# Kernel optimization log

Hardware: AMD Instinct MI355X
Metric: run time of the kernel (lower is better)

Reference implementation:

```python
import jax, jax.numpy as jnp
import numpy as np

B, T, C, I, E, K, V, H = 4, 512, 512, 2048, 32, 2, 32000, 8
D = C // H
EPS = 1e-5


def setup_inputs() -> dict:
    key = jax.random.key(0)
    ks = jax.random.split(key, 16)
    s = 0.02
    inp = {
        "input_ids": jax.random.randint(ks[0], (B, T), 0, V),
        "emb": jax.random.normal(ks[1], (V, C), jnp.float32) * s,
        "wq": jax.random.normal(ks[2], (C, C), jnp.float32) * s,
        "wk": jax.random.normal(ks[3], (C, C), jnp.float32) * s,
        "wv": jax.random.normal(ks[4], (C, C), jnp.float32) * s,
        "wo": jax.random.normal(ks[5], (C, C), jnp.float32) * s,
        "gate": jax.random.normal(ks[6], (C, E), jnp.float32) * s,
        "w1": jax.random.normal(ks[7], (E, C, I), jnp.float32) * s,
        "w2": jax.random.normal(ks[8], (E, I, C), jnp.float32) * s,
        "g1": jnp.ones((C,), jnp.float32) + jax.random.normal(ks[9], (C,), jnp.float32) * 0.01,
        "b1": jax.random.normal(ks[10], (C,), jnp.float32) * 0.01,
        "g2": jnp.ones((C,), jnp.float32) + jax.random.normal(ks[11], (C,), jnp.float32) * 0.01,
        "b2": jax.random.normal(ks[12], (C,), jnp.float32) * 0.01,
        "lm_head": jax.random.normal(ks[13], (C, V), jnp.float32) * s,
    }
    return inp


def _ln(x, g, b):
    mu = jnp.mean(x, axis=-1, keepdims=True)
    var = jnp.mean(jnp.square(x - mu), axis=-1, keepdims=True)
    return (x - mu) * jax.lax.rsqrt(var + EPS) * g + b


def reference(input_ids, emb, wq, wk, wv, wo, gate, w1, w2, g1, b1, g2, b2, lm_head):
    h = emb[input_ids]  # [B,T,C]
    # --- attention block ---
    x = _ln(h, g1, b1)
    q = (x @ wq).reshape(B, T, H, D).transpose(0, 2, 1, 3)  # [B,H,T,D]
    k = (x @ wk).reshape(B, T, H, D).transpose(0, 2, 1, 3)
    v = (x @ wv).reshape(B, T, H, D).transpose(0, 2, 1, 3)
    scores = jnp.einsum('bhqd,bhkd->bhqk', q, k) / jnp.sqrt(jnp.float32(D))
    causal = jnp.tril(jnp.ones((T, T), bool))
    scores = jnp.where(causal, scores, jnp.finfo(scores.dtype).min)
    attn = jax.nn.softmax(scores, axis=-1)
    ao = jnp.einsum('bhqk,bhkd->bhqd', attn, v)
    ao = ao.transpose(0, 2, 1, 3).reshape(B, T, C) @ wo
    h = h + ao
    # --- MoE block ---
    x2 = _ln(h, g2, b2)          # hidden_states_for_moe [B,T,C]
    flat = x2.reshape(-1, C)     # [N,C], N = B*T tokens
    router_logits = flat @ gate  # [N,E]
    rw, sel = jax.lax.top_k(router_logits, K)   # [N,K]
    rw = jax.nn.softmax(rw.astype(jnp.float32), axis=-1)
    # dense per-expert FFN, then mask to selected experts (same math as
    # torch's loop: unselected (token,expert) slots stay zero)
    hidden = jax.nn.gelu(jnp.einsum('tc,eci->tei', flat, w1), approximate=False)
    all_out = jnp.einsum('tei,eic->tec', hidden, w2)  # [N,E,C]
    sel_mask = jnp.sum(jax.nn.one_hot(sel, E, dtype=all_out.dtype), axis=1)  # [N,E]
    full_expert_outputs = all_out * sel_mask[:, :, None]
    gathered = jnp.take_along_axis(full_expert_outputs, sel[:, :, None], axis=1)  # [N,K,C]
    moe_out = jnp.einsum('tk,tkc->tc', rw, gathered).reshape(B, T, C)
    h = h + moe_out
    logits = h @ lm_head
    return logits, full_expert_outputs, router_logits, x2
```

## Files before the change

kernel.cpp:

```cpp
#include <hip/hip_runtime.h>
#include <hip/hip_bf16.h>

#define BATCH 4
#define SEQ   512
#define CH    512
#define NTOK  2048
#define FF    2048
#define NEXP  32
#define TOPK  2
#define VOCAB 32000
#define NHEAD 8
#define HDIM  64
#define EPSF  1e-5f

typedef __attribute__((ext_vector_type(8))) short short8v;
typedef __attribute__((ext_vector_type(4))) float f32x4;

#define GLD16(g, lds) __builtin_amdgcn_global_load_lds(                      \
    (const __attribute__((address_space(1))) void*)(g),                      \
    (__attribute__((address_space(3))) void*)(lds), 16, 0, 0)

__device__ __forceinline__ unsigned short bf16r(float f) {
  unsigned int u = __float_as_uint(f);
  u = (u + 0x7FFFu + ((u >> 16) & 1u)) >> 16;
  return (unsigned short)u;
}

__device__ __forceinline__ float block_reduce_sum(float v, float* sbuf) {
  #pragma unroll
  for (int off = 32; off > 0; off >>= 1) v += __shfl_down(v, off, 64);
  const int lane = threadIdx.x & 63, wid = threadIdx.x >> 6;
  __syncthreads();
  if (lane == 0) sbuf[wid] = v;
  __syncthreads();
  return sbuf[0] + sbuf[1] + sbuf[2] + sbuf[3];
}

__device__ __forceinline__ float gelu_exact(float v) {
  return 0.5f * v * (1.f + erff(v * 0.70710678118654752f));
}

__global__ __launch_bounds__(256) void transpose_cvt_kernel(
    const float* __restrict__ in, unsigned short* __restrict__ out, int R, int C) {
  __shared__ float T[64][65];
  const size_t zoff = (size_t)blockIdx.z * R * C;
  in += zoff; out += zoff;
  const int r0 = blockIdx.y << 6;
  const int c0 = blockIdx.x << 6;
  const int t = threadIdx.x;
  const int lr = t >> 4;
  const int lc = (t & 15) << 2;
  #pragma unroll
  for (int rr = 0; rr < 64; rr += 16) {
    const float4 v = *(const float4*)(in + (size_t)(r0 + lr + rr) * C + c0 + lc);
    T[lr + rr][lc + 0] = v.x; T[lr + rr][lc + 1] = v.y;
    T[lr + rr][lc + 2] = v.z; T[lr + rr][lc + 3] = v.w;
  }
  __syncthreads();
  const int oc = t >> 2;
  const int rs = (t & 3) << 4;
  unsigned int pk[8];
  #pragma unroll
  for (int j = 0; j < 8; ++j) {
    const float a = T[rs + 2 * j][oc];
    const float b = T[rs + 2 * j + 1][oc];
    pk[j] = (unsigned int)bf16r(a) | ((unsigned int)bf16r(b) << 16);
  }
  unsigned short* op = out + (size_t)(c0 + oc) * R + r0 + rs;
  *(uint4*)(op)     = make_uint4(pk[0], pk[1], pk[2], pk[3]);
  *(uint4*)(op + 8) = make_uint4(pk[4], pk[5], pk[6], pk[7]);
}

__global__ __launch_bounds__(256) void embed_ln_kernel(
    const int* __restrict__ ids, const float* __restrict__ emb,
    const float* __restrict__ g, const float* __restrict__ b,
    float* __restrict__ h, float* __restrict__ x) {
  __shared__ float sbuf[4];
  const int n = blockIdx.x, t = threadIdx.x;
  const float2 v = *(const float2*)(emb + (size_t)ids[n] * CH + 2 * t);
  *(float2*)(h + (size_t)n * CH + 2 * t) = v;
  const float mu = block_reduce_sum(v.x + v.y, sbuf) * (1.f / CH);
  const float d0 = v.x - mu, d1 = v.y - mu;
  const float var = block_reduce_sum(d0 * d0 + d1 * d1, sbuf) * (1.f / CH);
  const float rstd = rsqrtf(var + EPSF);
  const float2 gg = *(const float2*)(g + 2 * t);
  const float2 bb = *(const float2*)(b + 2 * t);
  *(float2*)(x + (size_t)n * CH + 2 * t) =
      make_float2(d0 * rstd * gg.x + bb.x, d1 * rstd * gg.y + bb.y);
}

__global__ __launch_bounds__(256) void ln2_router_kernel(
    const float* __restrict__ in, const float* __restrict__ g,
    const float* __restrict__ b, const float* __restrict__ gate,
    float* __restrict__ outf, unsigned short* __restrict__ outbf,
    float* __restrict__ rl, float* __restrict__ rw, int* __restrict__ sel,
    int* __restrict__ counts, int* __restrict__ lists) {
  __shared__ float sbuf[4];
  __shared__ float xrow[CH];
  __shared__ float lg[NEXP];
  const int n = blockIdx.x, t = threadIdx.x;
  const float2 v = *(const float2*)(in + (size_t)n * CH + 2 * t);
  const float mu = block_reduce_sum(v.x + v.y, sbuf) * (1.f / CH);
  const float d0 = v.x - mu, d1 = v.y - mu;
  const float var = block_reduce_sum(d0 * d0 + d1 * d1, sbuf) * (1.f / CH);
  const float rstd = rsqrtf(var + EPSF);
  const float2 gg = *(const float2*)(g + 2 * t);
  const float2 bb = *(const float2*)(b + 2 * t);
  const float o0 = d0 * rstd * gg.x + bb.x;
  const float o1 = d1 * rstd * gg.y + bb.y;
  *(float2*)(outf + (size_t)n * CH + 2 * t) = make_float2(o0, o1);
  ((unsigned int*)outbf)[(size_t)n * (CH / 2) + t] =
      (unsigned int)bf16r(o0) | ((unsigned int)bf16r(o1) << 16);
  xrow[2 * t] = o0; xrow[2 * t + 1] = o1;
  __syncthreads();
  const int e = t >> 3, i = t & 7;
  float p = 0.f;
  const float* gp = gate + e;
  for (int c = i * 64; c < i * 64 + 64; ++c) p = fmaf(xrow[c], gp[(size_t)c * NEXP], p);
  p += __shfl_xor(p, 1, 64);
  p += __shfl_xor(p, 2, 64);
  p += __shfl_xor(p, 4, 64);
  if (i == 0) { lg[e] = p; rl[(size_t)n * NEXP + e] = p; }
  __syncthreads();
  if (t == 0) {
    int i0 = 0; float v0 = lg[0];
    for (int j = 1; j < NEXP; ++j) if (lg[j] > v0) { v0 = lg[j]; i0 = j; }
    int i1 = (i0 == 0) ? 1 : 0; float v1 = lg[i1];
    for (int j = 0; j < NEXP; ++j) {
      if (j == i0 || j == i1) continue;
      if (lg[j] > v1) { v1 = lg[j]; i1 = j; }
    }
    const float ex = expf(v1 - v0);
    const float den = 1.f + ex;
    rw[n * 2]     = 1.f / den;
    rw[n * 2 + 1] = ex / den;
    sel[n * 2]     = i0;
    sel[n * 2 + 1] = i1;
    const int s0 = atomicAdd(&counts[i0], 1);
    lists[i0 * NTOK + s0] = n * 2;
    const int s1 = atomicAdd(&counts[i1], 1);
    lists[i1 * NTOK + s1] = n * 2 + 1;
  }
}

__global__ __launch_bounds__(256) void gemm_f32_qkv_kernel(
    const float* __restrict__ A,
    const float* __restrict__ Wq, const float* __restrict__ Wk,
    const float* __restrict__ Wv,
    float* __restrict__ Oq, float* __restrict__ Ok, float* __restrict__ Ov,
    int M, int N, int K) {
  const float* B = (blockIdx.z == 0) ? Wq : (blockIdx.z == 1) ? Wk : Wv;
  float*       C = (blockIdx.z == 0) ? Oq : (blockIdx.z == 1) ? Ok : Ov;
  __shared__ float As[32][68];
  __shared__ float Bs[32][132];
  const int m0 = blockIdx.y << 6;
  const int n0 = blockIdx.x << 7;
  const int t  = threadIdx.x;
  const int tm = t >> 4;
  const int tn = t & 15;
  float acc[4][8];
  #pragma unroll
  for (int i = 0; i < 4; ++i)
    #pragma unroll
    for (int j = 0; j < 8; ++j) acc[i][j] = 0.f;

  const int ar = t >> 3;
  const int ac = (t & 7) << 2;
  const int bk = t >> 3;
  const int bn = (t & 7) << 4;

  for (int kt = 0; kt < K; kt += 32) {
    #pragma unroll
    for (int rr = 0; rr < 64; rr += 32) {
      float4 a = *(const float4*)(A + (size_t)(m0 + ar + rr) * K + kt + ac);
      As[ac + 0][ar + rr] = a.x; As[ac + 1][ar + rr] = a.y;
      As[ac + 2][ar + rr] = a.z; As[ac + 3][ar + rr] = a.w;
    }
    const float* bp = B + (size_t)(kt + bk) * N + n0 + bn;
    #pragma unroll
    for (int j = 0; j < 16; j += 4)
      *(float4*)&Bs[bk][bn + j] = *(const float4*)(bp + j);
    __syncthreads();
    #pragma unroll
    for (int k = 0; k < 32; ++k) {
      const float4 av = *(const float4*)&As[k][tm << 2];
      const float4 bl = *(const float4*)&Bs[k][tn << 2];
      const float4 bh = *(const float4*)&Bs[k][64 + (tn << 2)];
      const float a_[4] = {av.x, av.y, av.z, av.w};
      const float b_[8] = {bl.x, bl.y, bl.z, bl.w, bh.x, bh.y, bh.z, bh.w};
      #pragma unroll
      for (int i = 0; i < 4; ++i)
        #pragma unroll
        for (int j = 0; j < 8; ++j)
          acc[i][j] = fmaf(a_[i], b_[j], acc[i][j]);
    }
    __syncthreads();
  }
  #pragma unroll
  for (int i = 0; i < 4; ++i) {
    const int row = m0 + (tm << 2) + i;
    float* cp = C + (size_t)row * N + n0 + (tn << 2);
    *(float4*)cp        = make_float4(acc[i][0], acc[i][1], acc[i][2], acc[i][3]);
    *(float4*)(cp + 64) = make_float4(acc[i][4], acc[i][5], acc[i][6], acc[i][7]);
  }
}

__global__ __launch_bounds__(256) void gemm_f32_kernel(
    const float* __restrict__ A, const float* __restrict__ B,
    const float* __restrict__ Res, float* __restrict__ C,
    int M, int N, int K) {
  __shared__ float As[32][68];
  __shared__ float Bs[32][132];
  const int m0 = blockIdx.y << 6;
  const int n0 = blockIdx.x << 7;
  const int t  = threadIdx.x;
  const int tm = t >> 4;
  const int tn = t & 15;
  float acc[4][8];
  #pragma unroll
  for (int i = 0; i < 4; ++i)
    #pragma unroll
    for (int j = 0; j < 8; ++j) acc[i][j] = 0.f;

  const int ar = t >> 3;
  const int ac = (t & 7) << 2;
  const int bk = t >> 3;
  const int bn = (t & 7) << 4;

  for (int kt = 0; kt < K; kt += 32) {
    #pragma unroll
    for (int rr = 0; rr < 64; rr += 32) {
      float4 a = *(const float4*)(A + (size_t)(m0 + ar + rr) * K + kt + ac);
      As[ac + 0][ar + rr] = a.x; As[ac + 1][ar + rr] = a.y;
      As[ac + 2][ar + rr] = a.z; As[ac + 3][ar + rr] = a.w;
    }
    const float* bp = B + (size_t)(kt + bk) * N + n0 + bn;
    #pragma unroll
    for (int j = 0; j < 16; j += 4)
      *(float4*)&Bs[bk][bn + j] = *(const float4*)(bp + j);
    __syncthreads();
    #pragma unroll
    for (int k = 0; k < 32; ++k) {
      const float4 av = *(const float4*)&As[k][tm << 2];
      const float4 bl = *(const float4*)&Bs[k][tn << 2];
      const float4 bh = *(const float4*)&Bs[k][64 + (tn << 2)];
      const float a_[4] = {av.x, av.y, av.z, av.w};
      const float b_[8] = {bl.x, bl.y, bl.z, bl.w, bh.x, bh.y, bh.z, bh.w};
      #pragma unroll
      for (int i = 0; i < 4; ++i)
        #pragma unroll
        for (int j = 0; j < 8; ++j)
          acc[i][j] = fmaf(a_[i], b_[j], acc[i][j]);
    }
    __syncthreads();
  }
  #pragma unroll
  for (int i = 0; i < 4; ++i) {
    const int row = m0 + (tm << 2) + i;
    float* cp = C + (size_t)row * N + n0 + (tn << 2);
    float4 lo = make_float4(acc[i][0], acc[i][1], acc[i][2], acc[i][3]);
    float4 hi = make_float4(acc[i][4], acc[i][5], acc[i][6], acc[i][7]);
    if (Res) {
      const float* rp = Res + (size_t)row * N + n0 + (tn << 2);
      const float4 r0 = *(const float4*)rp;
      const float4 r1 = *(const float4*)(rp + 64);
      lo.x += r0.x; lo.y += r0.y; lo.z += r0.z; lo.w += r0.w;
      hi.x += r1.x; hi.y += r1.y; hi.z += r1.z; hi.w += r1.w;
    }
    *(float4*)cp        = lo;
    *(float4*)(cp + 64) = hi;
  }
}

template <int SWZ>
__global__ __launch_bounds__(256) void gemm_bf16_kernel(
    const unsigned short* __restrict__ A, const unsigned short* __restrict__ BT,
    float* __restrict__ C, int M, int N, int K) {
  int bx = blockIdx.x, by = blockIdx.y;
  if (SWZ) {
    const int gx = gridDim.x;
    const int nb = gx * gridDim.y;
    int bid = by * gx + bx;
    bid = (bid & 7) * (nb >> 3) + (bid >> 3);
    bx = bid % gx;
    by = bid / gx;
  }
  __shared__ unsigned short As[128][64];
  __shared__ unsigned short Bs[128][64];
  __shared__ float Cs[4][16][68];
  const int m0 = by << 7;
  const int n0 = bx << 7;
  const int t  = threadIdx.x;
  const int w  = t >> 6;
  const int l  = t & 63;
  const int wm = (w >> 1) << 6;
  const int wn = (w & 1) << 6;
  const int fr = l & 15;
  const int fg = l >> 4;
  const int lrow = l >> 3;
  const int lcol = (l & 7) << 3;
  f32x4 acc[4][4];
  #pragma unroll
  for (int i = 0; i < 4; ++i)
    #pragma unroll
    for (int j = 0; j < 4; ++j) acc[i][j] = (f32x4){0.f, 0.f, 0.f, 0.f};

  for (int kt = 0; kt < K; kt += 64) {
    #pragma unroll
    for (int q = 0; q < 4; ++q) {
      const int r = (w << 5) + (q << 3);
      GLD16(A  + (size_t)(m0 + r + lrow) * K + kt + lcol, &As[r][0]);
      GLD16(BT + (size_t)(n0 + r + lrow) * K + kt + lcol, &Bs[r][0]);
    }
    __syncthreads();
    #pragma unroll
    for (int kk = 0; kk < 64; kk += 32) {
      short8v afr[4], bfr[4];
      #pragma unroll
      for (int i = 0; i < 4; ++i)
        afr[i] = *(const short8v*)&As[wm + (i << 4) + fr][kk + (fg << 3)];
      #pragma unroll
      for (int j = 0; j < 4; ++j)
        bfr[j] = *(const short8v*)&Bs[wn + (j << 4) + fr][kk + (fg << 3)];
      #pragma unroll
      for (int i = 0; i < 4; ++i)
        #pragma unroll
        for (int j = 0; j < 4; ++j)
          acc[i][j] = __builtin_amdgcn_mfma_f32_16x16x32_bf16(afr[i], bfr[j], acc[i][j], 0, 0, 0);
    }
    __syncthreads();
  }
  #pragma unroll
  for (int i = 0; i < 4; ++i) {
    #pragma unroll
    for (int j = 0; j < 4; ++j)
      #pragma unroll
      for (int r = 0; r < 4; ++r)
        Cs[w][(fg << 2) + r][(j << 4) + fr] = acc[i][j][r];
    __syncthreads();
    const int rr = l >> 2;
    const int cc = (l & 3) << 4;
    float* cp = C + (size_t)(m0 + wm + (i << 4) + rr) * N + n0 + wn + cc;
    *(float4*)(cp + 0)  = *(const float4*)&Cs[w][rr][cc + 0];
    *(float4*)(cp + 4)  = *(const float4*)&Cs[w][rr][cc + 4];
    *(float4*)(cp + 8)  = *(const float4*)&Cs[w][rr][cc + 8];
    *(float4*)(cp + 12) = *(const float4*)&Cs[w][rr][cc + 12];
    __syncthreads();
  }
}

__global__ __launch_bounds__(512) void attn_kernel(
    const float* __restrict__ q, const float* __restrict__ kbuf,
    const float* __restrict__ vbuf, float* __restrict__ ao) {
  __shared__ float Ks[64][68];
  __shared__ float Vs[64][68];
  __shared__ float Sx[64][65];
  const int bh = blockIdx.x;
  const int qt = blockIdx.y;
  const int b  = bh >> 3;
  const int hh = bh & 7;
  const int t  = threadIdx.x;
  const int qi   = t >> 3;
  const int part = t & 7;
  const int qglob = (qt << 6) + qi;
  const size_t qoff = (size_t)(b * SEQ + qglob) * CH + hh * HDIM + (part << 3);
  float qreg[8];
  {
    const float4 a = *(const float4*)(q + qoff);
    const float4 c = *(const float4*)(q + qoff + 4);
    qreg[0] = a.x; qreg[1] = a.y; qreg[2] = a.z; qreg[3] = a.w;
    qreg[4] = c.x; qreg[5] = c.y; qreg[6] = c.z; qreg[7] = c.w;
  }
  float o[8];
  #pragma unroll
  for (int j = 0; j < 8; ++j) o[j] = 0.f;
  float m = -3.0e38f, l = 0.f;
  const int lr = t >> 3;
  const int lc = (t & 7) << 3;
  for (int kt = 0; kt <= qt; ++kt) {
    const size_t base = (size_t)(b * SEQ + (kt << 6) + lr) * CH + hh * HDIM + lc;
    *(float4*)&Ks[lr][lc + 0] = *(const float4*)(kbuf + base + 0);
    *(float4*)&Ks[lr][lc + 4] = *(const float4*)(kbuf + base + 4);
    *(float4*)&Vs[lr][lc + 0] = *(const float4*)(vbuf + base + 0);
    *(float4*)&Vs[lr][lc + 4] = *(const float4*)(vbuf + base + 4);
    __syncthreads();
    float sloc[8];
    float tmax = -3.0e38f;
    for (int kk = 0; kk < 64; ++kk) {
      float p = 0.f;
      const float* kr = &Ks[kk][part << 3];
      #pragma unroll
      for (int j = 0; j < 8; ++j) p = fmaf(qreg[j], kr[j], p);
      p += __shfl_xor(p, 1, 64);
      p += __shfl_xor(p, 2, 64);
      p += __shfl_xor(p, 4, 64);
      p *= 0.125f;
      if (((kt << 6) + kk) > qglob) p = -3.0e38f;
      tmax = fmaxf(tmax, p);
      if ((kk & 7) == part) sloc[kk >> 3] = p;
    }
    const float mnew = fmaxf(m, tmax);
    const float corr = expf(m - mnew);
    float lsum = 0.f;
    #pragma unroll
    for (int j = 0; j < 8; ++j) {
      const float pe = expf(sloc[j] - mnew);
      lsum += pe;
      Sx[qi][(j << 3) + part] = pe;
    }
    lsum += __shfl_xor(lsum, 1, 64);
    lsum += __shfl_xor(lsum, 2, 64);
    lsum += __shfl_xor(lsum, 4, 64);
    l = l * corr + lsum;
    m = mnew;
    #pragma unroll
    for (int j = 0; j < 8; ++j) o[j] *= corr;
    for (int kk = 0; kk < 64; ++kk) {
      const float pv = Sx[qi][kk];
      const float* vr = &Vs[kk][part << 3];
      #pragma unroll
      for (int j = 0; j < 8; ++j) o[j] = fmaf(pv, vr[j], o[j]);
    }
    __syncthreads();
  }
  const float inv = 1.f / l;
  *(float4*)(ao + qoff)     = make_float4(o[0] * inv, o[1] * inv, o[2] * inv, o[3] * inv);
  *(float4*)(ao + qoff + 4) = make_float4(o[4] * inv, o[5] * inv, o[6] * inv, o[7] * inv);
}

__global__ __launch_bounds__(256) void moe_fc1_bf16(
    const unsigned short* __restrict__ x2bf, const unsigned short* __restrict__ w1T,
    const int* __restrict__ counts, const int* __restrict__ lists,
    unsigned short* __restrict__ hidden) {
  const int e  = blockIdx.y;
  const int nt = counts[e];
  const int mt = blockIdx.z << 6;
  if (mt >= nt) return;
  const int i0 = blockIdx.x << 7;
  __shared__ unsigned short As[64][72];
  __shared__ unsigned short Bs[128][64];
  __shared__ int ls[64];
  const int* lst = lists + e * NTOK;
  const int t = threadIdx.x;
  if (t < 64) ls[t] = (mt + t < nt) ? lst[mt + t] : -1;
  __syncthreads();
  const int w  = t >> 6, l = t & 63;
  const int wm = (w >> 1) << 5;
  const int wn = (w & 1) << 6;
  const int fr = l & 15, fg = l >> 4;
  const int lrow = l >> 3, lcol = (l & 7) << 3;
  f32x4 acc[2][4];
  #pragma unroll
  for (int i = 0; i < 2; ++i)
    #pragma unroll
    for (int j = 0; j < 4; ++j) acc[i][j] = (f32x4){0.f, 0.f, 0.f, 0.f};

  const int arow = t >> 2, akc = (t & 3) << 4;
  const int apid = ls[arow];
  const unsigned short* arp = (apid >= 0) ? (x2bf + (size_t)(apid >> 1) * CH) : nullptr;
  const unsigned short* w1e = w1T + (size_t)e * FF * CH;

  for (int kt = 0; kt < CH; kt += 64) {
    if (arp) {
      *(uint4*)&As[arow][akc + 0] = *(const uint4*)(arp + kt + akc + 0);
      *(uint4*)&As[arow][akc + 8] = *(const uint4*)(arp + kt + akc + 8);
    } else {
      *(uint4*)&As[arow][akc + 0] = make_uint4(0, 0, 0, 0);
      *(uint4*)&As[arow][akc + 8] = make_uint4(0, 0, 0, 0);
    }
    #pragma unroll
    for (int q = 0; q < 4; ++q) {
      const int r = (w << 5) + (q << 3);
      GLD16(w1e + (size_t)(i0 + r + lrow) * CH + kt + lcol, &Bs[r][0]);
    }
    __syncthreads();
    #pragma unroll
    for (int kk = 0; kk < 64; kk += 32) {
      short8v afr[2], bfr[4];
      #pragma unroll
      for (int i = 0; i < 2; ++i)
        afr[i] = *(const short8v*)&As[wm + (i << 4) + fr][kk + (fg << 3)];
      #pragma unroll
      for (int j = 0; j < 4; ++j)
        bfr[j] = *(const short8v*)&Bs[wn + (j << 4) + fr][kk + (fg << 3)];
      #pragma unroll
      for (int i = 0; i < 2; ++i)
        #pragma unroll
        for (int j = 0; j < 4; ++j)
          acc[i][j] = __builtin_amdgcn_mfma_f32_16x16x32_bf16(afr[i], bfr[j], acc[i][j], 0, 0, 0);
    }
    __syncthreads();
  }
  #pragma unroll
  for (int i = 0; i < 2; ++i) {
    #pragma unroll
    for (int r = 0; r < 4; ++r) {
      const int lrow2 = wm + (i << 4) + (fg << 2) + r;
      const int pid = ls[lrow2];
      if (pid < 0) continue;
      unsigned short* hp = hidden + (size_t)pid * FF + i0 + wn + fr;
      #pragma unroll
      for (int j = 0; j < 4; ++j)
        hp[j << 4] = bf16r(gelu_exact(acc[i][j][r]));
    }
  }
}

__global__ __launch_bounds__(256) void moe_fc2_bf16(
    const unsigned short* __restrict__ hidden, const unsigned short* __restrict__ w2T,
    const int* __restrict__ counts, const int* __restrict__ lists,
    float* __restrict__ fe) {
  const int e  = blockIdx.y;
  const int nt = counts[e];
  const int mt = blockIdx.z << 6;
  if (mt >= nt) return;
  const int c0 = blockIdx.x << 7;
  __shared__ unsigned short As[64][72];
  __shared__ unsigned short Bs[128][64];
  __shared__ int ls[64];
  const int* lst = lists + e * NTOK;
  const int t = threadIdx.x;
  if (t < 64) ls[t] = (mt + t < nt) ? lst[mt + t] : -1;
  __syncthreads();
  const int w  = t >> 6, l = t & 63;
  const int wm = (w >> 1) << 5;
  const int wn = (w & 1) << 6;
  const int fr = l & 15, fg = l >> 4;
  const int lrow = l >> 3, lcol = (l & 7) << 3;
  f32x4 acc[2][4];
  #pragma unroll
  for (int i = 0; i < 2; ++i)
    #pragma unroll
    for (int j = 0; j < 4; ++j) acc[i][j] = (f32x4){0.f, 0.f, 0.f, 0.f};

  const int arow = t >> 2, akc = (t & 3) << 4;
  const int apid = ls[arow];
  const unsigned short* arp = (apid >= 0) ? (hidden + (size_t)apid * FF) : nullptr;
  const unsigned short* w2e = w2T + (size_t)e * CH * FF;

  for (int kt = 0; kt < FF; kt += 64) {
    if (arp) {
      *(uint4*)&As[arow][akc + 0] = *(const uint4*)(arp + kt + akc + 0);
      *(uint4*)&As[arow][akc + 8] = *(const uint4*)(arp + kt + akc + 8);
    } else {
      *(uint4*)&As[arow][akc + 0] = make_uint4(0, 0, 0, 0);
      *(uint4*)&As[arow][akc + 8] = make_uint4(0, 0, 0, 0);
    }
    #pragma unroll
    for (int q = 0; q < 4; ++q) {
      const int r = (w << 5) + (q << 3);
      GLD16(w2e + (size_t)(c0 + r + lrow) * FF + kt + lcol, &Bs[r][0]);
    }
    __syncthreads();
    #pragma unroll
    for (int kk = 0; kk < 64; kk += 32) {
      short8v afr[2], bfr[4];
      #pragma unroll
      for (int i = 0; i < 2; ++i)
        afr[i] = *(const short8v*)&As[wm + (i << 4) + fr][kk + (fg << 3)];
      #pragma unroll
      for (int j = 0; j < 4; ++j)
        bfr[j] = *(const short8v*)&Bs[wn + (j << 4) + fr][kk + (fg << 3)];
      #pragma unroll
      for (int i = 0; i < 2; ++i)
        #pragma unroll
        for (int j = 0; j < 4; ++j)
          acc[i][j] = __builtin_amdgcn_mfma_f32_16x16x32_bf16(afr[i], bfr[j], acc[i][j], 0, 0, 0);
    }
    __syncthreads();
  }
  #pragma unroll
  for (int i = 0; i < 2; ++i) {
    #pragma unroll
    for (int r = 0; r < 4; ++r) {
      const int lrow2 = wm + (i << 4) + (fg << 2) + r;
      const int pid = ls[lrow2];
      if (pid < 0) continue;
      const int n = pid >> 1;
      float* op = fe + ((size_t)n * NEXP + e) * CH + c0 + wn + fr;
      #pragma unroll
      for (int j = 0; j < 4; ++j)
        op[j << 4] = acc[i][j][r];
    }
  }
}

__global__ __launch_bounds__(256) void combine_kernel(
    const float* __restrict__ h2, const float* __restrict__ fe,
    const float* __restrict__ rw, const int* __restrict__ sel,
    unsigned short* __restrict__ hfbf) {
  const int idx = blockIdx.x * 256 + threadIdx.x;
  const int n = idx >> 7;
  const int c = (idx & 127) << 2;
  const float w0 = rw[n * 2], w1 = rw[n * 2 + 1];
  const int s0 = sel[n * 2], s1 = sel[n * 2 + 1];
  const float* base = fe + (size_t)n * NEXP * CH + c;
  const float4 f0 = *(const float4*)(base + (size_t)s0 * CH);
  const float4 f1 = *(const float4*)(base + (size_t)s1 * CH);
  const float4 a  = *(const float4*)(h2 + (size_t)n * CH + c);
  const float ox = a.x + w0 * f0.x + w1 * f1.x;
  const float oy = a.y + w0 * f0.y + w1 * f1.y;
  const float oz = a.z + w0 * f0.z + w1 * f1.z;
  const float ow = a.w + w0 * f0.w + w1 * f1.w;
  uint2 pk;
  pk.x = (unsigned int)bf16r(ox) | ((unsigned int)bf16r(oy) << 16);
  pk.y = (unsigned int)bf16r(oz) | ((unsigned int)bf16r(ow) << 16);
  *(uint2*)(hfbf + (size_t)n * CH + c) = pk;
}

extern "C" void kernel_launch(void* const* d_in, const int* in_sizes, int n_in,
                              void* d_out, int out_size, void* d_ws, size_t ws_size,
                              hipStream_t stream) {
  const int*   ids  = (const int*)d_in[0];
  const float* emb  = (const float*)d_in[1];
  const float* wq   = (const float*)d_in[2];
  const float* wk   = (const float*)d_in[3];
  const float* wv   = (const float*)d_in[4];
  const float* wo   = (const float*)d_in[5];
  const float* gate = (const float*)d_in[6];
  const float* w1   = (const float*)d_in[7];
  const float* w2   = (const float*)d_in[8];
  const float* g1   = (const float*)d_in[9];
  const float* b1   = (const float*)d_in[10];
  const float* g2   = (const float*)d_in[11];
  const float* b2   = (const float*)d_in[12];
  const float* lmh  = (const float*)d_in[13];

  float* out        = (float*)d_out;
  float* out_logits = out;
  float* out_fe     = out_logits + (size_t)NTOK * VOCAB;
  float* out_rl     = out_fe + (size_t)NTOK * NEXP * CH;
  float* out_x2     = out_rl + (size_t)NTOK * NEXP;

  unsigned short* w1T    = (unsigned short*)(out_logits);
  unsigned short* w2T    = (unsigned short*)(out_logits + 16777216);
  unsigned short* hidden = (unsigned short*)(out_logits + 33554432);
  float*          x      = out_logits + 37748736;
  float*          qb     = out_logits + 38797312;
  float*          kb     = out_logits + 39845888;
  float*          vb     = out_logits + 40894464;
  float*          ao     = out_logits + 41943040;
  float*          h      = out_logits + 42991616;
  float*          h2     = out_logits + 44040192;
  unsigned short* x2_bf  = (unsigned short*)(out_logits + 45088768);

  float* ws    = (float*)d_ws;
  unsigned short* lmhT  = (unsigned short*)ws;
  unsigned short* hf_bf = (unsigned short*)(ws + 8192000);
  float* rw    = ws + 8716288;
  int*   sel   = (int*)(rw + NTOK * TOPK);
  int*   counts= sel + NTOK * TOPK;
  int*   lists = counts + 64;

  hipMemsetAsync(counts, 0, NEXP * sizeof(int), stream);
  hipMemsetAsync(out_fe, 0, (size_t)NTOK * NEXP * CH * sizeof(float), stream);

  transpose_cvt_kernel<<<dim3(500, 8, 1),   256, 0, stream>>>(lmh, lmhT, CH, VOCAB);
  transpose_cvt_kernel<<<dim3(32, 8, NEXP), 256, 0, stream>>>(w1, w1T, CH, FF);
  transpose_cvt_kernel<<<dim3(8, 32, NEXP), 256, 0, stream>>>(w2, w2T, FF, CH);

  embed_ln_kernel<<<NTOK, 256, 0, stream>>>(ids, emb, g1, b1, h, x);

  gemm_f32_qkv_kernel<<<dim3(CH / 128, NTOK / 64, 3), 256, 0, stream>>>(
      x, wq, wk, wv, qb, kb, vb, NTOK, CH, CH);

  attn_kernel<<<dim3(BATCH * NHEAD, SEQ / 64), 512, 0, stream>>>(qb, kb, vb, ao);

  gemm_f32_kernel<<<dim3(CH / 128, NTOK / 64), 256, 0, stream>>>(ao, wo, h, h2, NTOK, CH, CH);

  ln2_router_kernel<<<NTOK, 256, 0, stream>>>(h2, g2, b2, gate, out_x2, x2_bf,
                                              out_rl, rw, sel, counts, lists);

  moe_fc1_bf16<<<dim3(FF / 128, NEXP, NTOK / 64), 256, 0, stream>>>(x2_bf, w1T, counts, lists, hidden);
  moe_fc2_bf16<<<dim3(CH / 128, NEXP, NTOK / 64), 256, 0, stream>>>(hidden, w2T, counts, lists, out_fe);

  combine_kernel<<<dim3(NTOK * CH / 1024), 256, 0, stream>>>(h2, out_fe, rw, sel, hf_bf);

  gemm_bf16_kernel<1><<<dim3(VOCAB / 128, NTOK / 128), 256, 0, stream>>>(
      hf_bf, lmhT, out_logits, NTOK, VOCAB, CH);
}
```

Measured before the change: 1.178 ms.

## Double-buffer attention K/V, enlarge MoE GEMM tiles, drop LDS epilogue in LM-head GEMM

The attention kernel now prefetches the next K/V tile into registers while the current tile is processed and writes it into a second LDS buffer, which removes one barrier per iteration. The MoE fc1/fc2 kernels grow their token tile from 64 to 128 rows (4x4 MFMA accumulators per wave), which raises weight reuse at the cost of more registers and more padded rows for experts with few tokens. The bf16 LM-head GEMM writes accumulators straight to global memory instead of staging them through LDS, trading coalesced float4 stores for fewer barriers and less LDS use.

```diff
diff --git a/kernel.cpp b/kernel.cpp
--- a/kernel.cpp
+++ b/kernel.cpp
@@ -287,7 +287,6 @@
   }
   __shared__ unsigned short As[128][64];
   __shared__ unsigned short Bs[128][64];
-  __shared__ float Cs[4][16][68];
   const int m0 = by << 7;
   const int n0 = bx << 7;
   const int t  = threadIdx.x;
@@ -333,27 +332,21 @@
   #pragma unroll
   for (int i = 0; i < 4; ++i) {
     #pragma unroll
-    for (int j = 0; j < 4; ++j)
+    for (int j = 0; j < 4; ++j) {
+      const int col = n0 + wn + (j << 4) + fr;
+      const int rowb = m0 + wm + (i << 4) + (fg << 2);
       #pragma unroll
       for (int r = 0; r < 4; ++r)
-        Cs[w][(fg << 2) + r][(j << 4) + fr] = acc[i][j][r];
-    __syncthreads();
-    const int rr = l >> 2;
-    const int cc = (l & 3) << 4;
-    float* cp = C + (size_t)(m0 + wm + (i << 4) + rr) * N + n0 + wn + cc;
-    *(float4*)(cp + 0)  = *(const float4*)&Cs[w][rr][cc + 0];
-    *(float4*)(cp + 4)  = *(const float4*)&Cs[w][rr][cc + 4];
-    *(float4*)(cp + 8)  = *(const float4*)&Cs[w][rr][cc + 8];
-    *(float4*)(cp + 12) = *(const float4*)&Cs[w][rr][cc + 12];
-    __syncthreads();
+        C[(size_t)(rowb + r) * N + col] = acc[i][j][r];
+    }
   }
 }
 
 __global__ __launch_bounds__(512) void attn_kernel(
     const float* __restrict__ q, const float* __restrict__ kbuf,
     const float* __restrict__ vbuf, float* __restrict__ ao) {
-  __shared__ float Ks[64][68];
-  __shared__ float Vs[64][68];
+  __shared__ float K0[64][68], K1[64][68];
+  __shared__ float V0[64][68], V1[64][68];
   __shared__ float Sx[64][65];
   const int bh = blockIdx.x;
   const int qt = blockIdx.y;
@@ -377,13 +370,26 @@
   float m = -3.0e38f, l = 0.f;
   const int lr = t >> 3;
   const int lc = (t & 7) << 3;
+  {
+    const size_t base = (size_t)(b * SEQ + lr) * CH + hh * HDIM + lc;
+    *(float4*)&K0[lr][lc + 0] = *(const float4*)(kbuf + base + 0);
+    *(float4*)&K0[lr][lc + 4] = *(const float4*)(kbuf + base + 4);
+    *(float4*)&V0[lr][lc + 0] = *(const float4*)(vbuf + base + 0);
+    *(float4*)&V0[lr][lc + 4] = *(const float4*)(vbuf + base + 4);
+  }
+  __syncthreads();
   for (int kt = 0; kt <= qt; ++kt) {
-    const size_t base = (size_t)(b * SEQ + (kt << 6) + lr) * CH + hh * HDIM + lc;
-    *(float4*)&Ks[lr][lc + 0] = *(const float4*)(kbuf + base + 0);
-    *(float4*)&Ks[lr][lc + 4] = *(const float4*)(kbuf + base + 4);
-    *(float4*)&Vs[lr][lc + 0] = *(const float4*)(vbuf + base + 0);
-    *(float4*)&Vs[lr][lc + 4] = *(const float4*)(vbuf + base + 4);
-    __syncthreads();
+    const int cur = kt & 1;
+    float4 ka, kc, va, vc;
+    if (kt < qt) {
+      const size_t nb = (size_t)(b * SEQ + ((kt + 1) << 6) + lr) * CH + hh * HDIM + lc;
+      ka = *(const float4*)(kbuf + nb + 0);
+      kc = *(const float4*)(kbuf + nb + 4);
+      va = *(const float4*)(vbuf + nb + 0);
+      vc = *(const float4*)(vbuf + nb + 4);
+    }
+    const float (*Ks)[68] = cur ? K1 : K0;
+    const float (*Vs)[68] = cur ? V1 : V0;
     float sloc[8];
     float tmax = -3.0e38f;
     for (int kk = 0; kk < 64; ++kk) {
@@ -421,6 +427,14 @@
       #pragma unroll
       for (int j = 0; j < 8; ++j) o[j] = fmaf(pv, vr[j], o[j]);
     }
+    if (kt < qt) {
+      float (*Kn)[68] = cur ? K0 : K1;
+      float (*Vn)[68] = cur ? V0 : V1;
+      *(float4*)&Kn[lr][lc + 0] = ka;
+      *(float4*)&Kn[lr][lc + 4] = kc;
+      *(float4*)&Vn[lr][lc + 0] = va;
+      *(float4*)&Vn[lr][lc + 4] = vc;
+    }
     __syncthreads();
   }
   const float inv = 1.f / l;
@@ -434,39 +448,41 @@
     unsigned short* __restrict__ hidden) {
   const int e  = blockIdx.y;
   const int nt = counts[e];
-  const int mt = blockIdx.z << 6;
+  const int mt = blockIdx.z << 7;
   if (mt >= nt) return;
   const int i0 = blockIdx.x << 7;
-  __shared__ unsigned short As[64][72];
+  __shared__ unsigned short As[128][72];
   __shared__ unsigned short Bs[128][64];
-  __shared__ int ls[64];
+  __shared__ int ls[128];
   const int* lst = lists + e * NTOK;
   const int t = threadIdx.x;
-  if (t < 64) ls[t] = (mt + t < nt) ? lst[mt + t] : -1;
+  if (t < 128) ls[t] = (mt + t < nt) ? lst[mt + t] : -1;
   __syncthreads();
   const int w  = t >> 6, l = t & 63;
-  const int wm = (w >> 1) << 5;
+  const int wm = (w >> 1) << 6;
   const int wn = (w & 1) << 6;
   const int fr = l & 15, fg = l >> 4;
   const int lrow = l >> 3, lcol = (l & 7) << 3;
-  f32x4 acc[2][4];
-  #pragma unroll
-  for (int i = 0; i < 2; ++i)
+  f32x4 acc[4][4];
+  #pragma unroll
+  for (int i = 0; i < 4; ++i)
     #pragma unroll
     for (int j = 0; j < 4; ++j) acc[i][j] = (f32x4){0.f, 0.f, 0.f, 0.f};
 
-  const int arow = t >> 2, akc = (t & 3) << 4;
+  const int arow = t >> 1, akc = (t & 1) << 5;
   const int apid = ls[arow];
   const unsigned short* arp = (apid >= 0) ? (x2bf + (size_t)(apid >> 1) * CH) : nullptr;
   const unsigned short* w1e = w1T + (size_t)e * FF * CH;
 
   for (int kt = 0; kt < CH; kt += 64) {
     if (arp) {
-      *(uint4*)&As[arow][akc + 0] = *(const uint4*)(arp + kt + akc + 0);
-      *(uint4*)&As[arow][akc + 8] = *(const uint4*)(arp + kt + akc + 8);
+      #pragma unroll
+      for (int s = 0; s < 4; ++s)
+        *(uint4*)&As[arow][akc + (s << 3)] = *(const uint4*)(arp + kt + akc + (s << 3));
     } else {
-      *(uint4*)&As[arow][akc + 0] = make_uint4(0, 0, 0, 0);
-      *(uint4*)&As[arow][akc + 8] = make_uint4(0, 0, 0, 0);
+      #pragma unroll
+      for (int s = 0; s < 4; ++s)
+        *(uint4*)&As[arow][akc + (s << 3)] = make_uint4(0, 0, 0, 0);
     }
     #pragma unroll
     for (int q = 0; q < 4; ++q) {
@@ -476,15 +492,15 @@
     __syncthreads();
     #pragma unroll
     for (int kk = 0; kk < 64; kk += 32) {
-      short8v afr[2], bfr[4];
-      #pragma unroll
-      for (int i = 0; i < 2; ++i)
+      short8v afr[4], bfr[4];
+      #pragma unroll
+      for (int i = 0; i < 4; ++i)
         afr[i] = *(const short8v*)&As[wm + (i << 4) + fr][kk + (fg << 3)];
       #pragma unroll
       for (int j = 0; j < 4; ++j)
         bfr[j] = *(const short8v*)&Bs[wn + (j << 4) + fr][kk + (fg << 3)];
       #pragma unroll
-      for (int i = 0; i < 2; ++i)
+      for (int i = 0; i < 4; ++i)
         #pragma unroll
         for (int j = 0; j < 4; ++j)
           acc[i][j] = __builtin_amdgcn_mfma_f32_16x16x32_bf16(afr[i], bfr[j], acc[i][j], 0, 0, 0);
@@ -492,7 +508,7 @@
     __syncthreads();
   }
   #pragma unroll
-  for (int i = 0; i < 2; ++i) {
+  for (int i = 0; i < 4; ++i) {
     #pragma unroll
     for (int r = 0; r < 4; ++r) {
       const int lrow2 = wm + (i << 4) + (fg << 2) + r;
@@ -512,39 +528,41 @@
     float* __restrict__ fe) {
   const int e  = blockIdx.y;
   const int nt = counts[e];
-  const int mt = blockIdx.z << 6;
+  const int mt = blockIdx.z << 7;
   if (mt >= nt) return;
   const int c0 = blockIdx.x << 7;
-  __shared__ unsigned short As[64][72];
+  __shared__ unsigned short As[128][72];
   __shared__ unsigned short Bs[128][64];
-  __shared__ int ls[64];
+  __shared__ int ls[128];
   const int* lst = lists + e * NTOK;
   const int t = threadIdx.x;
-  if (t < 64) ls[t] = (mt + t < nt) ? lst[mt + t] : -1;
+  if (t < 128) ls[t] = (mt + t < nt) ? lst[mt + t] : -1;
   __syncthreads();
   const int w  = t >> 6, l = t & 63;
-  const int wm = (w >> 1) << 5;
+  const int wm = (w >> 1) << 6;
   const int wn = (w & 1) << 6;
   const int fr = l & 15, fg = l >> 4;
   const int lrow = l >> 3, lcol = (l & 7) << 3;
-  f32x4 acc[2][4];
-  #pragma unroll
-  for (int i = 0; i < 2; ++i)
+  f32x4 acc[4][4];
+  #pragma unroll
+  for (int i = 0; i < 4; ++i)
     #pragma unroll
     for (int j = 0; j < 4; ++j) acc[i][j] = (f32x4){0.f, 0.f, 0.f, 0.f};
 
-  const int arow = t >> 2, akc = (t & 3) << 4;
+  const int arow = t >> 1, akc = (t & 1) << 5;
   const int apid = ls[arow];
   const unsigned short* arp = (apid >= 0) ? (hidden + (size_t)apid * FF) : nullptr;
   const unsigned short* w2e = w2T + (size_t)e * CH * FF;
 
   for (int kt = 0; kt < FF; kt += 64) {
     if (arp) {
-      *(uint4*)&As[arow][akc + 0] = *(const uint4*)(arp + kt + akc + 0);
-      *(uint4*)&As[arow][akc + 8] = *(const uint4*)(arp + kt + akc + 8);
+      #pragma unroll
+      for (int s = 0; s < 4; ++s)
+        *(uint4*)&As[arow][akc + (s << 3)] = *(const uint4*)(arp + kt + akc + (s << 3));
     } else {
-      *(uint4*)&As[arow][akc + 0] = make_uint4(0, 0, 0, 0);
-      *(uint4*)&As[arow][akc + 8] = make_uint4(0, 0, 0, 0);
+      #pragma unroll
+      for (int s = 0; s < 4; ++s)
+        *(uint4*)&As[arow][akc + (s << 3)] = make_uint4(0, 0, 0, 0);
     }
     #pragma unroll
     for (int q = 0; q < 4; ++q) {
@@ -554,15 +572,15 @@
     __syncthreads();
     #pragma unroll
     for (int kk = 0; kk < 64; kk += 32) {
-      short8v afr[2], bfr[4];
-      #pragma unroll
-      for (int i = 0; i < 2; ++i)
+      short8v afr[4], bfr[4];
+      #pragma unroll
+      for (int i = 0; i < 4; ++i)
         afr[i] = *(const short8v*)&As[wm + (i << 4) + fr][kk + (fg << 3)];
       #pragma unroll
       for (int j = 0; j < 4; ++j)
         bfr[j] = *(const short8v*)&Bs[wn + (j << 4) + fr][kk + (fg << 3)];
       #pragma unroll
-      for (int i = 0; i < 2; ++i)
+      for (int i = 0; i < 4; ++i)
         #pragma unroll
         for (int j = 0; j < 4; ++j)
           acc[i][j] = __builtin_amdgcn_mfma_f32_16x16x32_bf16(afr[i], bfr[j], acc[i][j], 0, 0, 0);
@@ -570,7 +588,7 @@
     __syncthreads();
   }
   #pragma unroll
-  for (int i = 0; i < 2; ++i) {
+  for (int i = 0; i < 4; ++i) {
     #pragma unroll
     for (int r = 0; r < 4; ++r) {
       const int lrow2 = wm + (i << 4) + (fg << 2) + r;
@@ -671,8 +689,8 @@
   ln2_router_kernel<<<NTOK, 256, 0, stream>>>(h2, g2, b2, gate, out_x2, x2_bf,
                                               out_rl, rw, sel, counts, lists);
 
-  moe_fc1_bf16<<<dim3(FF / 128, NEXP, NTOK / 64), 256, 0, stream>>>(x2_bf, w1T, counts, lists, hidden);
-  moe_fc2_bf16<<<dim3(CH / 128, NEXP, NTOK / 64), 256, 0, stream>>>(hidden, w2T, counts, lists, out_fe);
+  moe_fc1_bf16<<<dim3(FF / 128, NEXP, NTOK / 128), 256, 0, stream>>>(x2_bf, w1T, counts, lists, hidden);
+  moe_fc2_bf16<<<dim3(CH / 128, NEXP, NTOK / 128), 256, 0, stream>>>(hidden, w2T, counts, lists, out_fe);
 
   combine_kernel<<<dim3(NTOK * CH / 1024), 256, 0, stream>>>(h2, out_fe, rw, sel, hf_bf);
 
```

Result: slower. 1.657 ms (+40.7%).
